# Kernel optimization log

Measured on AMD Instinct MI355X. Metric: run time of the kernel, lower is better.

Reference implementation:

```python
import jax, jax.numpy as jnp
import numpy as np

B, T, DQ, DF, H, D = 64, 4096, 512, 256, 8, 64
EPS = 1e-7

def setup_inputs() -> dict:
    key = jax.random.key(0)
    ks = jax.random.split(key, 6)
    return {
        "query": jax.random.normal(ks[0], (B, 1, DQ), dtype=jnp.float32),
        "fact": jax.random.normal(ks[1], (B, T, DF), dtype=jnp.float32),
        "Wq": jax.random.normal(ks[2], (H, DQ, D), dtype=jnp.float32) / np.sqrt(DQ).astype(np.float32),
        "bq": jax.random.normal(ks[3], (H, D), dtype=jnp.float32) * 0.1,
        "Wf": jax.random.normal(ks[4], (H, DF, D), dtype=jnp.float32) / np.sqrt(DF).astype(np.float32),
        "bf": jax.random.normal(ks[5], (H, D), dtype=jnp.float32) * 0.1,
    }

def reference(query, fact, Wq, bq, Wf, bf):
    # Per-head linear projections, batched over the head axis h.
    # fc_query: [B, H, 1, D]; fc_fact: [B, H, T, D]
    fq = jnp.einsum('bqf,hfd->bhqd', query, Wq) + bq[None, :, None, :]
    ff = jnp.einsum('btf,hfd->bhtd', fact, Wf) + bf[None, :, None, :]
    # dot = fc_fact @ fc_query^T -> [B, H, T, 1]
    dot = jnp.einsum('bhtd,bhqd->bhtq', ff, fq)
    # softmax over the sequence (torch dim=1 of [B, T, 1]) + epsilon
    alphas = jax.nn.softmax(dot, axis=2) + EPS
    # out_k = fc_fact^T @ alphas -> [B, H, D, 1]; concat heads on dim 1, squeeze dim 2
    out = jnp.einsum('bhtd,bhtq->bhdq', ff, alphas)
    return out.reshape(out.shape[0], H * D)
```

## Files before the change

### kernel.cpp

```cpp
#include <hip/hip_runtime.h>
#include <hip/hip_bf16.h>

#define B_ 64
#define T_ 4096
#define DQ_ 512
#define DF_ 256
#define H_ 8
#define D_ 64
#define EPS_ 1e-7f
#define NBLK 512
#define CHUNK 32
#define NCH 16
#define PS_STRIDE 2304
#define ROWB 1040
#define SLOTS 2080
#define BUFB (SLOTS * 16)

typedef __attribute__((ext_vector_type(8))) short short8;
typedef __attribute__((ext_vector_type(4))) float f32x4;

union U8 { uint4 u; short8 s; };

#if defined(__has_builtin)
#if __has_builtin(__builtin_amdgcn_global_load_lds)
#define HAVE_GLL 1
#endif
#endif

#ifdef HAVE_GLL
static __device__ __forceinline__ void STAGE16(const void* g, void* l) {
  __builtin_amdgcn_global_load_lds(
      (const __attribute__((address_space(1))) unsigned int*)g,
      (__attribute__((address_space(3))) unsigned int*)l, 16, 0, 0);
}
#else
static __device__ __forceinline__ void STAGE16(const void* g, void* l) {
  *(float4*)l = *(const float4*)g;
}
#endif

static __device__ __forceinline__ unsigned int pk2(float a, float b) {
  __hip_bfloat162 h = __float22bfloat162_rn(make_float2(a, b));
  union { __hip_bfloat162 h; unsigned int u; } c; c.h = h;
  return c.u;
}

__global__ __launch_bounds__(256) void prep(const float* __restrict__ qin,
    const float* __restrict__ Wq, const float* __restrict__ bq,
    const float* __restrict__ Wf, unsigned short* __restrict__ vB) {
  __shared__ float qs[DQ_];
  __shared__ float red[4][D_];
  __shared__ float fql[D_];
  int bh = blockIdx.x, b = bh >> 3, h = bh & 7;
  int tid = threadIdx.x, d = tid & 63, fc = tid >> 6;
  qs[tid] = qin[(size_t)b * DQ_ + tid];
  qs[tid + 256] = qin[(size_t)b * DQ_ + tid + 256];
  __syncthreads();
  {
    const float* w = Wq + (size_t)h * DQ_ * D_ + (size_t)fc * 128 * D_ + d;
    float acc = 0.f;
#pragma unroll 8
    for (int i = 0; i < 128; ++i) acc += qs[fc * 128 + i] * w[(size_t)i * D_];
    red[fc][d] = acc;
  }
  __syncthreads();
  if (fc == 0)
    fql[d] = red[0][d] + red[1][d] + red[2][d] + red[3][d] + bq[h * D_ + d];
  __syncthreads();
  const float4* wr = (const float4*)(Wf + (size_t)h * DF_ * D_ + (size_t)tid * D_);
  const float4* f4 = (const float4*)fql;
  float acc = 0.f;
#pragma unroll
  for (int i = 0; i < 16; ++i) {
    float4 wv = wr[i], fv = f4[i];
    acc += wv.x * fv.x + wv.y * fv.y + wv.z * fv.z + wv.w * fv.w;
  }
  int ks = tid >> 5, kg = (tid >> 3) & 3, j = tid & 7;
  size_t base = (size_t)b * 4096 + ks * 512;
  vB[base + (kg * 16 + h) * 8 + j] = (unsigned short)(pk2(acc, 0.f) & 0xFFFF);
  vB[base + (kg * 16 + 8 + h) * 8 + j] = 0;
}

__global__ __launch_bounds__(256, 2) void mha_main(
    const float* __restrict__ fact, const unsigned short* __restrict__ vB,
    float* __restrict__ part_s, float* __restrict__ part_ml) {
  __shared__ char buf[2 * BUFB];
  __shared__ float4 exch[2][4][64];

  const int tid = threadIdx.x;
  const int l = tid & 63, w = tid >> 6;
  const int dl = l & 15, kg = l >> 4;
  const int bid = blockIdx.x;
  const int b = bid >> 3, qq = bid & 7;

  short8 vfrag[2];
#pragma unroll
  for (int ks = 0; ks < 2; ++ks)
    vfrag[ks] = *(const short8*)(vB + (size_t)b * 4096 + (2 * w + ks) * 512 + l * 8);

  const float* factb = fact + ((size_t)b * T_ + (size_t)qq * 512) * DF_;

  int srow[9], sslot[9];
#pragma unroll
  for (int i = 0; i < 9; ++i) {
    int id = i * 256 + tid;
    int rho = id / 65;
    int kgr = (rho >> 3) & 3;
    srow[i] = (rho & ~7) | (((rho & 7) + 8 - 2 * kgr) & 7);
    sslot[i] = id % 65;
  }

  const int t0 = dl, t1 = 16 + dl;
  const int lr0 = (t0 & ~7) | (((t0 & 7) + 2 * ((t0 >> 3) & 3)) & 7);
  const int lr1 = (t1 & ~7) | (((t1 & 7) + 2 * ((t1 >> 3) & 3)) & 7);
  const int aoff0 = lr0 * ROWB + (w * 64 + kg * 8) * 4;
  const int aoff1 = lr1 * ROWB + (w * 64 + kg * 8) * 4;
  int roff[8];
#pragma unroll
  for (int j = 0; j < 8; ++j)
    roff[j] = (kg * 8 + ((j + 2 * kg) & 7)) * ROWB;

#define ISSUE(C) {                                                            \
    const char* gsrc = (const char*)(factb + (size_t)(C) * CHUNK * DF_);      \
    char* ldst = buf + ((C) & 1) * BUFB;                                      \
    _Pragma("unroll") for (int i = 0; i < 9; ++i) {                           \
      int id = i * 256 + tid;                                                 \
      if (i < 8 || id < SLOTS) {                                              \
        const void* sp = (sslot[i] < 64)                                      \
            ? (const void*)(gsrc + (size_t)srow[i] * 1024 + sslot[i] * 16)    \
            : (const void*)gsrc;                                              \
        STAGE16(sp, (void*)(ldst + id * 16));                                 \
      } } }

  float m_run = -INFINITY, l_part = 0.f;
  f32x4 acc_s[4];
#pragma unroll
  for (int n = 0; n < 4; ++n) { f32x4 z = {0.f, 0.f, 0.f, 0.f}; acc_s[n] = z; }

  ISSUE(0);

  for (int c = 0; c < NCH; ++c) {
    __syncthreads();
    const char* bc = buf + (c & 1) * BUFB;

    f32x4 dp[2];
#pragma unroll
    for (int t2 = 0; t2 < 2; ++t2) {
      const char* arow = bc + (t2 ? aoff1 : aoff0);
      float4 a0 = *(const float4*)arow;
      float4 a1 = *(const float4*)(arow + 16);
      float4 a2 = *(const float4*)(arow + 128);
      float4 a3 = *(const float4*)(arow + 144);
      U8 af0, af1;
      af0.u.x = pk2(a0.x, a0.y); af0.u.y = pk2(a0.z, a0.w);
      af0.u.z = pk2(a1.x, a1.y); af0.u.w = pk2(a1.z, a1.w);
      af1.u.x = pk2(a2.x, a2.y); af1.u.y = pk2(a2.z, a2.w);
      af1.u.z = pk2(a3.x, a3.y); af1.u.w = pk2(a3.z, a3.w);
      f32x4 d_ = {0.f, 0.f, 0.f, 0.f};
      d_ = __builtin_amdgcn_mfma_f32_16x16x32_bf16(af0.s, vfrag[0], d_, 0, 0, 0);
      d_ = __builtin_amdgcn_mfma_f32_16x16x32_bf16(af1.s, vfrag[1], d_, 0, 0, 0);
      dp[t2] = d_;
      exch[t2][w][l] = make_float4(d_[0], d_[1], d_[2], d_[3]);
    }
    __syncthreads();

    if (c + 1 < NCH) ISSUE(c + 1);

    f32x4 l0 = dp[0], l1 = dp[1];
#pragma unroll
    for (int ww = 1; ww < 4; ++ww) {
      int o = (w + ww) & 3;
      float4 p0 = exch[0][o][l], p1 = exch[1][o][l];
      l0[0] += p0.x; l0[1] += p0.y; l0[2] += p0.z; l0[3] += p0.w;
      l1[0] += p1.x; l1[1] += p1.y; l1[2] += p1.z; l1[3] += p1.w;
    }

    float tmax = fmaxf(fmaxf(fmaxf(l0[0], l0[1]), fmaxf(l0[2], l0[3])),
                       fmaxf(fmaxf(l1[0], l1[1]), fmaxf(l1[2], l1[3])));
    tmax = fmaxf(tmax, __shfl_xor(tmax, 16));
    tmax = fmaxf(tmax, __shfl_xor(tmax, 32));
    int need = (tmax > m_run + 8.f) && (dl < 8);
    if (__any(need)) {
      float mnew = fmaxf(m_run, tmax);
      float f = __expf(m_run - mnew);
      m_run = mnew;
      l_part *= f;
      float f0 = __shfl(f, kg * 4 + 0), f1 = __shfl(f, kg * 4 + 1);
      float f2 = __shfl(f, kg * 4 + 2), f3 = __shfl(f, kg * 4 + 3);
      if (kg < 2) {
#pragma unroll
        for (int n = 0; n < 4; ++n) {
          acc_s[n][0] *= f0; acc_s[n][1] *= f1; acc_s[n][2] *= f2; acc_s[n][3] *= f3;
        }
      }
    }
    float e0 = __expf(l0[0] - m_run), e1 = __expf(l0[1] - m_run);
    float e2 = __expf(l0[2] - m_run), e3 = __expf(l0[3] - m_run);
    float e4 = __expf(l1[0] - m_run), e5 = __expf(l1[1] - m_run);
    float e6 = __expf(l1[2] - m_run), e7 = __expf(l1[3] - m_run);
    l_part += (e0 + e1 + e2 + e3) + (e4 + e5 + e6 + e7);

    unsigned int pk00 = pk2(e0, e1), pk01 = pk2(e2, e3);
    unsigned int pk10 = pk2(e4, e5), pk11 = pk2(e6, e7);
    if (dl == 8) { pk00 = pk01 = pk10 = pk11 = 0x3F803F80u; }

    int sa = dl + ((kg & 1) ? 32 : 0);
    int sb = sa + 16;
    unsigned int g00 = __shfl(pk00, sa), g01 = __shfl(pk01, sa);
    unsigned int g02 = __shfl(pk00, sb), g03 = __shfl(pk01, sb);
    unsigned int g10 = __shfl(pk10, sa), g11 = __shfl(pk11, sa);
    unsigned int g12 = __shfl(pk10, sb), g13 = __shfl(pk11, sb);
    U8 eA;
    eA.u.x = (kg < 2) ? g00 : g10;
    eA.u.y = (kg < 2) ? g01 : g11;
    eA.u.z = (kg < 2) ? g02 : g12;
    eA.u.w = (kg < 2) ? g03 : g13;

#pragma unroll
    for (int n = 0; n < 4; ++n) {
      const char* srd = bc + (size_t)(w * 64 + n * 16 + dl) * 4;
      float b0 = *(const float*)(srd + roff[0]);
      float b1 = *(const float*)(srd + roff[1]);
      float b2 = *(const float*)(srd + roff[2]);
      float b3 = *(const float*)(srd + roff[3]);
      float b4 = *(const float*)(srd + roff[4]);
      float b5 = *(const float*)(srd + roff[5]);
      float b6 = *(const float*)(srd + roff[6]);
      float b7 = *(const float*)(srd + roff[7]);
      U8 bb;
      bb.u.x = pk2(b0, b1); bb.u.y = pk2(b2, b3);
      bb.u.z = pk2(b4, b5); bb.u.w = pk2(b6, b7);
      acc_s[n] = __builtin_amdgcn_mfma_f32_16x16x32_bf16(eA.s, bb.s, acc_s[n], 0, 0, 0);
    }
  }

  l_part += __shfl_xor(l_part, 16);
  l_part += __shfl_xor(l_part, 32);
  if (w == 0 && l < 8) {
    part_ml[(size_t)bid * 16 + l] = m_run;
    part_ml[(size_t)bid * 16 + 8 + l] = l_part;
  }
  float* ps = part_s + (size_t)bid * PS_STRIDE;
  if (kg < 2) {
#pragma unroll
    for (int n = 0; n < 4; ++n) {
      int f = w * 64 + n * 16 + dl;
      ps[(kg * 4 + 0) * 256 + f] = acc_s[n][0];
      ps[(kg * 4 + 1) * 256 + f] = acc_s[n][1];
      ps[(kg * 4 + 2) * 256 + f] = acc_s[n][2];
      ps[(kg * 4 + 3) * 256 + f] = acc_s[n][3];
    }
  } else if (kg == 2) {
#pragma unroll
    for (int n = 0; n < 4; ++n)
      ps[8 * 256 + w * 64 + n * 16 + dl] = acc_s[n][0];
  }
}

__global__ __launch_bounds__(256) void reduce_k(const float* __restrict__ part_s,
    const float* __restrict__ part_ml, const float* __restrict__ Wf,
    const float* __restrict__ bf, float* __restrict__ out) {
  __shared__ float s_l[DF_];
  __shared__ float red[4][D_];
  int bh = blockIdx.x, b = bh >> 3, h = bh & 7;
  int tid = threadIdx.x, d = tid & 63, fc = tid >> 6;
  float M = -INFINITY;
  float mq[8];
#pragma unroll
  for (int q = 0; q < 8; ++q) {
    mq[q] = part_ml[(size_t)(b * 8 + q) * 16 + h];
    M = fmaxf(M, mq[q]);
  }
  float L = 0.f, sa = 0.f, cs = 0.f;
#pragma unroll
  for (int q = 0; q < 8; ++q) {
    float e = __expf(mq[q] - M);
    L += e * part_ml[(size_t)(b * 8 + q) * 16 + 8 + h];
    const float* ps = part_s + (size_t)(b * 8 + q) * PS_STRIDE;
    sa += e * ps[h * 256 + tid];
    cs += ps[8 * 256 + tid];
  }
  s_l[tid] = sa / L + EPS_ * cs;
  __syncthreads();
  const float* wbase = Wf + (size_t)h * DF_ * D_ + (size_t)fc * 64 * D_ + d;
  float o = 0.f;
#pragma unroll 8
  for (int k = 0; k < 64; ++k) o += s_l[fc * 64 + k] * wbase[(size_t)k * D_];
  red[fc][d] = o;
  __syncthreads();
  if (fc == 0)
    out[(size_t)b * (H_ * D_) + h * D_ + d] =
        o + red[1][d] + red[2][d] + red[3][d] + (1.f + (float)T_ * EPS_) * bf[h * D_ + d];
}

extern "C" void kernel_launch(void* const* d_in, const int* in_sizes, int n_in,
                              void* d_out, int out_size, void* d_ws, size_t ws_size,
                              hipStream_t stream) {
  const float* query = (const float*)d_in[0];
  const float* fact  = (const float*)d_in[1];
  const float* Wq    = (const float*)d_in[2];
  const float* bq    = (const float*)d_in[3];
  const float* Wf    = (const float*)d_in[4];
  const float* bf    = (const float*)d_in[5];
  float* out = (float*)d_out;

  char* ws = (char*)d_ws;
  unsigned short* vB = (unsigned short*)ws;
  float* part_ml = (float*)(ws + 524288);
  float* part_s = (float*)(ws + 557056);

  prep<<<dim3(B_ * H_), dim3(256), 0, stream>>>(query, Wq, bq, Wf, vB);
  mha_main<<<dim3(NBLK), dim3(256), 0, stream>>>(fact, vB, part_s, part_ml);
  reduce_k<<<dim3(B_ * H_), dim3(256), 0, stream>>>(part_s, part_ml, Wf, bf, out);
}
```

Measured before the change: 68.80 us.

## Triple-buffer fact staging with explicit vmcnt waits and batch prep over 8 batches

The main kernel moves from double to triple buffering of fact chunks in LDS, prefetching two chunks ahead. It replaces __syncthreads with explicit s_waitcnt vmcnt/lgkmcnt plus raw s_barrier, so loads of later chunks stay in flight across barriers. LDS use grows to three buffers and launch bounds drop to one block per CU-slot hint, which may reduce occupancy. Separately, the prep kernel now handles 8 batches per block so each Wq/Wf weight load is reused across batches, with 64 blocks instead of 512.

```diff
diff --git a/kernel.cpp b/kernel.cpp
--- a/kernel.cpp
+++ b/kernel.cpp
@@ -48,43 +48,55 @@
 __global__ __launch_bounds__(256) void prep(const float* __restrict__ qin,
     const float* __restrict__ Wq, const float* __restrict__ bq,
     const float* __restrict__ Wf, unsigned short* __restrict__ vB) {
-  __shared__ float qs[DQ_];
-  __shared__ float red[4][D_];
-  __shared__ float fql[D_];
-  int bh = blockIdx.x, b = bh >> 3, h = bh & 7;
-  int tid = threadIdx.x, d = tid & 63, fc = tid >> 6;
-  qs[tid] = qin[(size_t)b * DQ_ + tid];
-  qs[tid + 256] = qin[(size_t)b * DQ_ + tid + 256];
+  __shared__ float qs[8][DQ_];
+  __shared__ float fqs[8][D_];
+  int blk = blockIdx.x, h = blk >> 3, bg = blk & 7;
+  int tid = threadIdx.x;
+  int d = tid & 63, bp = tid >> 6;
+#pragma unroll
+  for (int bb = 0; bb < 8; ++bb) {
+    qs[bb][tid] = qin[(size_t)(bg * 8 + bb) * DQ_ + tid];
+    qs[bb][tid + 256] = qin[(size_t)(bg * 8 + bb) * DQ_ + tid + 256];
+  }
   __syncthreads();
   {
-    const float* w = Wq + (size_t)h * DQ_ * D_ + (size_t)fc * 128 * D_ + d;
-    float acc = 0.f;
+    const float* w = Wq + (size_t)h * DQ_ * D_ + d;
+    float a0 = 0.f, a1 = 0.f;
 #pragma unroll 8
-    for (int i = 0; i < 128; ++i) acc += qs[fc * 128 + i] * w[(size_t)i * D_];
-    red[fc][d] = acc;
-  }
-  __syncthreads();
-  if (fc == 0)
-    fql[d] = red[0][d] + red[1][d] + red[2][d] + red[3][d] + bq[h * D_ + d];
+    for (int f = 0; f < DQ_; ++f) {
+      float wv = w[(size_t)f * D_];
+      a0 += qs[bp * 2][f] * wv;
+      a1 += qs[bp * 2 + 1][f] * wv;
+    }
+    float bv = bq[h * D_ + d];
+    fqs[bp * 2][d] = a0 + bv;
+    fqs[bp * 2 + 1][d] = a1 + bv;
+  }
   __syncthreads();
   const float4* wr = (const float4*)(Wf + (size_t)h * DF_ * D_ + (size_t)tid * D_);
-  const float4* f4 = (const float4*)fql;
-  float acc = 0.f;
+  float acc[8] = {0.f, 0.f, 0.f, 0.f, 0.f, 0.f, 0.f, 0.f};
 #pragma unroll
   for (int i = 0; i < 16; ++i) {
-    float4 wv = wr[i], fv = f4[i];
-    acc += wv.x * fv.x + wv.y * fv.y + wv.z * fv.z + wv.w * fv.w;
+    float4 wv = wr[i];
+#pragma unroll
+    for (int bb = 0; bb < 8; ++bb) {
+      float4 fv = ((const float4*)&fqs[bb][0])[i];
+      acc[bb] += wv.x * fv.x + wv.y * fv.y + wv.z * fv.z + wv.w * fv.w;
+    }
   }
   int ks = tid >> 5, kg = (tid >> 3) & 3, j = tid & 7;
-  size_t base = (size_t)b * 4096 + ks * 512;
-  vB[base + (kg * 16 + h) * 8 + j] = (unsigned short)(pk2(acc, 0.f) & 0xFFFF);
-  vB[base + (kg * 16 + 8 + h) * 8 + j] = 0;
-}
-
-__global__ __launch_bounds__(256, 2) void mha_main(
+#pragma unroll
+  for (int bb = 0; bb < 8; ++bb) {
+    size_t base = (size_t)(bg * 8 + bb) * 4096 + ks * 512;
+    vB[base + (kg * 16 + h) * 8 + j] = (unsigned short)(pk2(acc[bb], 0.f) & 0xFFFF);
+    vB[base + (kg * 16 + 8 + h) * 8 + j] = 0;
+  }
+}
+
+__global__ __launch_bounds__(256, 1) void mha_main(
     const float* __restrict__ fact, const unsigned short* __restrict__ vB,
     float* __restrict__ part_s, float* __restrict__ part_ml) {
-  __shared__ char buf[2 * BUFB];
+  __shared__ char buf[3 * BUFB];
   __shared__ float4 exch[2][4][64];
 
   const int tid = threadIdx.x;
@@ -100,14 +112,22 @@
 
   const float* factb = fact + ((size_t)b * T_ + (size_t)qq * 512) * DF_;
 
-  int srow[9], sslot[9];
-#pragma unroll
-  for (int i = 0; i < 9; ++i) {
+  int srow[8], sslot[8];
+#pragma unroll
+  for (int i = 0; i < 8; ++i) {
     int id = i * 256 + tid;
     int rho = id / 65;
     int kgr = (rho >> 3) & 3;
     srow[i] = (rho & ~7) | (((rho & 7) + 8 - 2 * kgr) & 7);
     sslot[i] = id % 65;
+  }
+  const int id8 = 2048 + w * 8 + (l & 7);
+  int srow8, sslot8;
+  {
+    int rho = id8 / 65;
+    int kgr = (rho >> 3) & 3;
+    srow8 = (rho & ~7) | (((rho & 7) + 8 - 2 * kgr) & 7);
+    sslot8 = id8 % 65;
   }
 
   const int t0 = dl, t1 = 16 + dl;
@@ -122,15 +142,20 @@
 
 #define ISSUE(C) {                                                            \
     const char* gsrc = (const char*)(factb + (size_t)(C) * CHUNK * DF_);      \
-    char* ldst = buf + ((C) & 1) * BUFB;                                      \
-    _Pragma("unroll") for (int i = 0; i < 9; ++i) {                           \
+    char* ldst = buf + ((C) % 3) * BUFB;                                      \
+    _Pragma("unroll") for (int i = 0; i < 8; ++i) {                           \
       int id = i * 256 + tid;                                                 \
-      if (i < 8 || id < SLOTS) {                                              \
-        const void* sp = (sslot[i] < 64)                                      \
-            ? (const void*)(gsrc + (size_t)srow[i] * 1024 + sslot[i] * 16)    \
-            : (const void*)gsrc;                                              \
-        STAGE16(sp, (void*)(ldst + id * 16));                                 \
-      } } }
+      const void* sp = (sslot[i] < 64)                                        \
+          ? (const void*)(gsrc + (size_t)srow[i] * 1024 + sslot[i] * 16)      \
+          : (const void*)gsrc;                                                \
+      STAGE16(sp, (void*)(ldst + id * 16));                                   \
+    }                                                                         \
+    if (l < 8) {                                                              \
+      const void* sp = (sslot8 < 64)                                          \
+          ? (const void*)(gsrc + (size_t)srow8 * 1024 + sslot8 * 16)          \
+          : (const void*)gsrc;                                                \
+      STAGE16(sp, (void*)(ldst + id8 * 16));                                  \
+    } }
 
   float m_run = -INFINITY, l_part = 0.f;
   f32x4 acc_s[4];
@@ -138,10 +163,16 @@
   for (int n = 0; n < 4; ++n) { f32x4 z = {0.f, 0.f, 0.f, 0.f}; acc_s[n] = z; }
 
   ISSUE(0);
+  ISSUE(1);
 
   for (int c = 0; c < NCH; ++c) {
-    __syncthreads();
-    const char* bc = buf + (c & 1) * BUFB;
+    if (c == NCH - 1) { asm volatile("s_waitcnt vmcnt(0)" ::: "memory"); }
+    else { asm volatile("s_waitcnt vmcnt(9)" ::: "memory"); }
+    __builtin_amdgcn_sched_barrier(0);
+    __builtin_amdgcn_s_barrier();
+    __builtin_amdgcn_sched_barrier(0);
+
+    const char* bc = buf + (c % 3) * BUFB;
 
     f32x4 dp[2];
 #pragma unroll
@@ -162,9 +193,12 @@
       dp[t2] = d_;
       exch[t2][w][l] = make_float4(d_[0], d_[1], d_[2], d_[3]);
     }
-    __syncthreads();
-
-    if (c + 1 < NCH) ISSUE(c + 1);
+    asm volatile("s_waitcnt lgkmcnt(0)" ::: "memory");
+    __builtin_amdgcn_sched_barrier(0);
+    __builtin_amdgcn_s_barrier();
+    __builtin_amdgcn_sched_barrier(0);
+
+    if (c + 2 < NCH) ISSUE(c + 2);
 
     f32x4 l0 = dp[0], l1 = dp[1];
 #pragma unroll
@@ -309,7 +343,7 @@
   float* part_ml = (float*)(ws + 524288);
   float* part_s = (float*)(ws + 557056);
 
-  prep<<<dim3(B_ * H_), dim3(256), 0, stream>>>(query, Wq, bq, Wf, vB);
+  prep<<<dim3(64), dim3(256), 0, stream>>>(query, Wq, bq, Wf, vB);
   mha_main<<<dim3(NBLK), dim3(256), 0, stream>>>(fact, vB, part_s, part_ml);
   reduce_k<<<dim3(B_ * H_), dim3(256), 0, stream>>>(part_s, part_ml, Wf, bf, out);
 }
```

Result: slower. 95.99 us (+39.5%).
